# Kernel optimization log

Hardware: AMD Instinct MI355X
Metric: run time of the kernel (lower is better)

Reference implementation:

```python
import jax, jax.numpy as jnp
import numpy as np

N_NODES = 50000
N_EDGES = 1600000
F = 128
UNITS = 128


def leaky_relu2(x):
    # kgcnn>leaky_relu2: leaky relu with alpha=0.2
    return jnp.where(x > 0, x, 0.2 * x)


def glorot(key, shape):
    lim = np.sqrt(6.0 / (shape[0] + shape[1]))
    return jax.random.uniform(key, shape, jnp.float32, -lim, lim)


def setup_inputs() -> dict:
    key = jax.random.key(0)
    ks = jax.random.split(key, 8)
    node = jax.random.normal(ks[0], (N_NODES, F), jnp.float32)
    edge = jax.random.normal(ks[1], (N_EDGES, F), jnp.float32)
    edge_index = jax.random.randint(ks[2], (N_EDGES, 2), 0, N_NODES, jnp.int64)
    # lay_linear_trafo: Dense(units) on sender features
    W_lin = glorot(ks[3], (F, UNITS))
    b_lin = jnp.zeros((UNITS,), jnp.float32)
    # lay_alpha_activation: Dense(units, leaky_relu2) on concat [n_in || n_out]
    W_att = glorot(ks[4], (2 * F, UNITS))
    b_att = jnp.zeros((UNITS,), jnp.float32)
    # lay_alpha: Dense(1, linear, no bias)
    w_alpha = glorot(ks[5], (UNITS, 1))
    return {"node": node, "edge": edge, "edge_index": edge_index,
            "W_lin": W_lin, "b_lin": b_lin, "W_att": W_att, "b_att": b_att,
            "w_alpha": w_alpha}


def reference(node, edge, edge_index, W_lin, b_lin, W_att, b_att, w_alpha):
    recv = edge_index[:, 0]  # ingoing node i (receiver)
    send = edge_index[:, 1]  # outgoing node j (sender)
    n_in = node[recv]        # [M, F]
    n_out = node[send]       # [M, F]
    # linear trafo of sender features: W2 h_j
    wn_out = n_out @ W_lin + b_lin                       # [M, U]
    # attention logits a_ij = sigma1(W1 [h_i || h_j]) -> Dense(1)
    e_ij = leaky_relu2(jnp.concatenate([n_in, n_out], axis=-1) @ W_att + b_att)
    a_ij = (e_ij @ w_alpha)[:, 0]                        # [M]
    # segment softmax over edges incoming to each receiver node
    seg_max = jax.ops.segment_max(a_ij, recv, num_segments=N_NODES)
    seg_max = jnp.where(jnp.isfinite(seg_max), seg_max, 0.0)
    a_exp = jnp.exp(a_ij - seg_max[recv])
    denom = jax.ops.segment_sum(a_exp, recv, num_segments=N_NODES)
    alpha = a_exp / jnp.maximum(denom[recv], 1e-12)      # [M]
    # scatter weighted sum back to receiver nodes
    n_i = jax.ops.segment_sum(alpha[:, None] * wn_out, recv, num_segments=N_NODES)
    return jax.nn.elu(n_i)                               # [N, U]
```

## Files before the change

kernel.cpp:

```cpp
#include <hip/hip_runtime.h>
#include <hip/hip_bf16.h>
#include <math.h>

#define F 128
#define CAP 128

typedef __attribute__((ext_vector_type(8))) short bf16x8;
typedef __attribute__((ext_vector_type(4))) float f32x4;

static __device__ __forceinline__ unsigned short f2bf(float f) {
  unsigned u = __float_as_uint(f);
  unsigned r = (u + 0x7fffu + ((u >> 16) & 1u)) >> 16;
  return (unsigned short)r;
}
static __device__ __forceinline__ float bf2f(unsigned short h) {
  return __uint_as_float(((unsigned)h) << 16);
}

__global__ __launch_bounds__(256) void prep_kernel(
    const float* __restrict__ W_att, const float* __restrict__ W_lin,
    unsigned short* __restrict__ Bpack, int* __restrict__ deg, int nNodes) {
  const int i = blockIdx.x * 256 + threadIdx.x;
  if (i < nNodes) deg[i] = 0;
  if (i < 24 * 4 * 64 * 8) {
    const int j  = i & 7;
    const int l  = (i >> 3) & 63;
    const int kt = (i >> 9) & 3;
    const int ct = i >> 11;
    const int k = kt * 32 + ((l >> 4) << 3) + j;
    const int c = ct * 16 + (l & 15);
    float v;
    if (c < 128)      v = W_att[k * 128 + c];
    else if (c < 256) v = W_att[(k + 128) * 128 + (c - 128)];
    else              v = W_lin[k * 128 + (c - 256)];
    Bpack[i] = f2bf(v);
  }
}

static __device__ void gemm_body_mfma(
    int r0, const float* __restrict__ node,
    const unsigned short* __restrict__ Bpack,
    const float* __restrict__ b_att, const float* __restrict__ b_lin,
    float* __restrict__ A_in, unsigned short* __restrict__ P, int nNodes) {
  const int w   = threadIdx.x >> 6;
  const int l   = threadIdx.x & 63;
  const int l15 = l & 15;
  const int g   = l >> 4;

  const int rowA  = r0 + w * 16 + l15;
  const int rowAc = min(rowA, nNodes - 1);

  bf16x8 af[4];
  const float* arow = node + (size_t)rowAc * F + (g << 3);
#pragma unroll
  for (int kt = 0; kt < 4; ++kt) {
    const float4 x0 = *(const float4*)(arow + kt * 32);
    const float4 x1 = *(const float4*)(arow + kt * 32 + 4);
    bf16x8 a;
    a[0] = (short)f2bf(x0.x); a[1] = (short)f2bf(x0.y);
    a[2] = (short)f2bf(x0.z); a[3] = (short)f2bf(x0.w);
    a[4] = (short)f2bf(x1.x); a[5] = (short)f2bf(x1.y);
    a[6] = (short)f2bf(x1.z); a[7] = (short)f2bf(x1.w);
    af[kt] = a;
  }

  const int growBase = r0 + w * 16 + (g << 2);

  for (int ct = 0; ct < 24; ++ct) {
    f32x4 acc = {0.f, 0.f, 0.f, 0.f};
    const unsigned short* bp = Bpack + (((size_t)(ct * 4) * 64 + l) << 3);
#pragma unroll
    for (int kt = 0; kt < 4; ++kt) {
      const bf16x8 bfr = *(const bf16x8*)(bp + (kt << 9));
      acc = __builtin_amdgcn_mfma_f32_16x16x32_bf16(af[kt], bfr, acc, 0, 0, 0);
    }
    const int col = ct * 16 + l15;
#pragma unroll
    for (int r = 0; r < 4; ++r) {
      const int grow = growBase + r;
      if (grow < nNodes) {
        if (col < 128) {
          A_in[(size_t)grow * F + col] = acc[r] + b_att[col];
        } else if (col < 256) {
          P[(size_t)grow * 256 + (col - 128)] = f2bf(acc[r]);
        } else {
          P[(size_t)grow * 256 + 128 + (col - 256)] =
              f2bf(acc[r] + b_lin[col - 256]);
        }
      }
    }
  }
}

__global__ __launch_bounds__(256) void combo_kernel(
    const int2* __restrict__ ei2, int* __restrict__ deg,
    int* __restrict__ sorted_send, int nEdges, int SB,
    const float* __restrict__ node, const unsigned short* __restrict__ Bpack,
    const float* __restrict__ b_att, const float* __restrict__ b_lin,
    float* __restrict__ A_in, unsigned short* __restrict__ P, int nNodes) {
  if ((int)blockIdx.x < SB) {
    for (int e = (int)blockIdx.x * 256 + threadIdx.x; e < nEdges;
         e += SB * 256) {
      int2 p = ei2[e];
      int r = atomicAdd(&deg[p.x], 1);
      if (r < CAP) sorted_send[((size_t)p.x << 7) + r] = p.y;
    }
    return;
  }
  gemm_body_mfma((blockIdx.x - SB) * 64, node, Bpack, b_att, b_lin,
                 A_in, P, nNodes);
}

__global__ __launch_bounds__(256) void fused_node(
    const float* __restrict__ A_in, const unsigned short* __restrict__ P,
    const float* __restrict__ w_alpha, const int* __restrict__ deg,
    const int* __restrict__ sorted_send,
    float* __restrict__ out, int nNodes) {
  const int node = blockIdx.x * 4 + (threadIdx.x >> 6);
  const int lane = threadIdx.x & 63;
  if (node >= nNodes) return;

  const int e0 = node << 7;
  const int d  = min(deg[node], CAP);
  const int e1 = e0 + d;
  const int l31 = lane & 31;
  const int hi8 = (lane & 32) >> 2;
  const size_t no = (size_t)node * F;

  const float4 ai = *(const float4*)&A_in[no + (l31 << 2)];
  const float4 wa = *(const float4*)&w_alpha[l31 << 2];

  float4 acc = {0.f, 0.f, 0.f, 0.f};
  float pacc = 0.f;
  float tsave = 0.f;

  for (int base64 = e0; base64 < e1; base64 += 64) {
    const int myidx = (base64 + lane < e1) ? sorted_send[base64 + lane] : 0;
    const int rem = e1 - base64;
    const int nch = ((rem < 64 ? rem : 64) + 15) >> 4;
    for (int c = 0; c < nch; ++c) {
      const int base = base64 + c * 16;

      int srow[8];
      ushort4 qa[8], wb[8];
#pragma unroll
      for (int q = 0; q < 8; ++q) {
        srow[q] = __shfl(myidx, c * 16 + q + hi8);
        const unsigned short* rp = P + (size_t)srow[q] * 256 + (l31 << 2);
        qa[q] = *(const ushort4*)rp;
        wb[q] = *(const ushort4*)(rp + 128);
      }

#pragma unroll
      for (int q = 0; q < 8; ++q) {
        float x0 = bf2f(qa[q].x) + ai.x; x0 = fmaxf(x0, 0.2f * x0);
        float x1 = bf2f(qa[q].y) + ai.y; x1 = fmaxf(x1, 0.2f * x1);
        float x2 = bf2f(qa[q].z) + ai.z; x2 = fmaxf(x2, 0.2f * x2);
        float x3 = bf2f(qa[q].w) + ai.w; x3 = fmaxf(x3, 0.2f * x3);
        float s = fmaf(x0, wa.x, fmaf(x1, wa.y, fmaf(x2, wa.z, x3 * wa.w)));
        s += __shfl_xor(s, 1);
        s += __shfl_xor(s, 2);
        s += __shfl_xor(s, 4);
        s += __shfl_xor(s, 8);
        s += __shfl_xor(s, 16);
        tsave = (l31 == q) ? s : tsave;
      }

      const int edge = base + l31 + hi8;
      const float p = ((l31 < 8) && (edge < e1)) ? __expf(tsave) : 0.f;
      pacc += p;

#pragma unroll
      for (int q = 0; q < 8; ++q) {
        const float pq = __shfl(p, (lane & 32) + q);
        acc.x = fmaf(bf2f(wb[q].x), pq, acc.x);
        acc.y = fmaf(bf2f(wb[q].y), pq, acc.y);
        acc.z = fmaf(bf2f(wb[q].z), pq, acc.z);
        acc.w = fmaf(bf2f(wb[q].w), pq, acc.w);
      }
    }
  }

  acc.x += __shfl_xor(acc.x, 32);
  acc.y += __shfl_xor(acc.y, 32);
  acc.z += __shfl_xor(acc.z, 32);
  acc.w += __shfl_xor(acc.w, 32);
  for (int off = 1; off < 64; off <<= 1) pacc += __shfl_xor(pacc, off);

  const float inv = 1.f / fmaxf(pacc, 1e-12f);
  if (lane < 32) {
    float v0 = acc.x * inv, v1 = acc.y * inv, v2 = acc.z * inv, v3 = acc.w * inv;
    v0 = (v0 > 0.f) ? v0 : expm1f(v0);
    v1 = (v1 > 0.f) ? v1 : expm1f(v1);
    v2 = (v2 > 0.f) ? v2 : expm1f(v2);
    v3 = (v3 > 0.f) ? v3 : expm1f(v3);
    *(float4*)&out[no + (l31 << 2)] = float4{v0, v1, v2, v3};
  }
}

extern "C" void kernel_launch(void* const* d_in, const int* in_sizes, int n_in,
                              void* d_out, int out_size, void* d_ws, size_t ws_size,
                              hipStream_t stream) {
  const float* node    = (const float*)d_in[0];
  const int*   ei      = (const int*)d_in[2];
  const float* W_lin   = (const float*)d_in[3];
  const float* b_lin   = (const float*)d_in[4];
  const float* W_att   = (const float*)d_in[5];
  const float* b_att   = (const float*)d_in[6];
  const float* w_alpha = (const float*)d_in[7];

  const int nNodes = in_sizes[0] / F;
  const int nEdges = in_sizes[2] / 2;

  float* ws = (float*)d_ws;
  const size_t nf = (size_t)nNodes * F;
  float*          A_in = ws;
  unsigned short* P    = (unsigned short*)(ws + nf);
  int*            deg  = (int*)(ws + 2 * nf);
  int*  sorted_send    = deg + nNodes;
  unsigned short* Bpack =
      (unsigned short*)(sorted_send + (size_t)nNodes * CAP);

  const int PB = max((nNodes + 255) / 256, 192);
  const int SB = 768;
  const int GB = (nNodes + 63) / 64;
  const int NB = (nNodes + 3) / 4;

  prep_kernel<<<PB, 256, 0, stream>>>(W_att, W_lin, Bpack, deg, nNodes);
  combo_kernel<<<SB + GB, 256, 0, stream>>>(
      (const int2*)ei, deg, sorted_send, nEdges, SB,
      node, Bpack, b_att, b_lin, A_in, P, nNodes);
  fused_node<<<NB, 256, 0, stream>>>(
      A_in, P, w_alpha, deg, sorted_send, (float*)d_out, nNodes);
}
```

Baseline: 225.8 us.

## Double-buffer gathered edge rows in fused_node to overlap loads with compute

Restructures the per-node edge loop into a software pipeline with two register buffers. The next chunk's gathered P rows are issued before the current chunk's attention logits and weighted sum are computed. Both 64-index blocks of sorted_send are preloaded up front, replacing the nested 64/16 loop. This is meant to hide gather latency behind compute, at the cost of more registers and possibly lower occupancy.

Result: no change. 227.6 us (+0.8%).

```diff
diff --git a/kernel.cpp b/kernel.cpp
--- a/kernel.cpp
+++ b/kernel.cpp
@@ -122,7 +122,6 @@
 
   const int e0 = node << 7;
   const int d  = min(deg[node], CAP);
-  const int e1 = e0 + d;
   const int l31 = lane & 31;
   const int hi8 = (lane & 32) >> 2;
   const size_t no = (size_t)node * F;
@@ -133,53 +132,92 @@
   float4 acc = {0.f, 0.f, 0.f, 0.f};
   float pacc = 0.f;
   float tsave = 0.f;
-
-  for (int base64 = e0; base64 < e1; base64 += 64) {
-    const int myidx = (base64 + lane < e1) ? sorted_send[base64 + lane] : 0;
-    const int rem = e1 - base64;
-    const int nch = ((rem < 64 ? rem : 64) + 15) >> 4;
-    for (int c = 0; c < nch; ++c) {
-      const int base = base64 + c * 16;
-
-      int srow[8];
-      ushort4 qa[8], wb[8];
-#pragma unroll
-      for (int q = 0; q < 8; ++q) {
-        srow[q] = __shfl(myidx, c * 16 + q + hi8);
-        const unsigned short* rp = P + (size_t)srow[q] * 256 + (l31 << 2);
-        qa[q] = *(const ushort4*)rp;
-        wb[q] = *(const ushort4*)(rp + 128);
-      }
-
-#pragma unroll
-      for (int q = 0; q < 8; ++q) {
-        float x0 = bf2f(qa[q].x) + ai.x; x0 = fmaxf(x0, 0.2f * x0);
-        float x1 = bf2f(qa[q].y) + ai.y; x1 = fmaxf(x1, 0.2f * x1);
-        float x2 = bf2f(qa[q].z) + ai.z; x2 = fmaxf(x2, 0.2f * x2);
-        float x3 = bf2f(qa[q].w) + ai.w; x3 = fmaxf(x3, 0.2f * x3);
-        float s = fmaf(x0, wa.x, fmaf(x1, wa.y, fmaf(x2, wa.z, x3 * wa.w)));
-        s += __shfl_xor(s, 1);
-        s += __shfl_xor(s, 2);
-        s += __shfl_xor(s, 4);
-        s += __shfl_xor(s, 8);
-        s += __shfl_xor(s, 16);
-        tsave = (l31 == q) ? s : tsave;
-      }
-
-      const int edge = base + l31 + hi8;
-      const float p = ((l31 < 8) && (edge < e1)) ? __expf(tsave) : 0.f;
-      pacc += p;
-
-#pragma unroll
-      for (int q = 0; q < 8; ++q) {
-        const float pq = __shfl(p, (lane & 32) + q);
-        acc.x = fmaf(bf2f(wb[q].x), pq, acc.x);
-        acc.y = fmaf(bf2f(wb[q].y), pq, acc.y);
-        acc.z = fmaf(bf2f(wb[q].z), pq, acc.z);
-        acc.w = fmaf(bf2f(wb[q].w), pq, acc.w);
-      }
-    }
-  }
+  float p = 0.f;
+
+  const int myidx0 = (lane < d) ? sorted_send[e0 + lane] : 0;
+  const int myidx1 = (64 + lane < d) ? sorted_send[e0 + 64 + lane] : 0;
+
+  const int nch = (d + 15) >> 4;
+
+  ushort4 qaA[8], wbA[8], qaB[8], wbB[8];
+
+#define IDS(CH) (((CH) & 4) ? myidx1 : myidx0)
+
+#define ISSUE_QA(BUF, CH)                                              \
+  {                                                                    \
+    const int ids_ = IDS(CH);                                          \
+    _Pragma("unroll") for (int q = 0; q < 8; ++q) {                    \
+      const int srow = __shfl(ids_, ((CH) & 3) * 16 + q + hi8);        \
+      BUF[q] = *(const ushort4*)(P + (size_t)srow * 256 + (l31 << 2)); \
+    }                                                                  \
+  }
+
+#define ISSUE_WB(BUF, CH)                                              \
+  {                                                                    \
+    const int ids_ = IDS(CH);                                          \
+    _Pragma("unroll") for (int q = 0; q < 8; ++q) {                    \
+      const int srow = __shfl(ids_, ((CH) & 3) * 16 + q + hi8);        \
+      BUF[q] =                                                         \
+          *(const ushort4*)(P + (size_t)srow * 256 + 128 + (l31 << 2)); \
+    }                                                                  \
+  }
+
+#define PHASE_A(BUF, CH)                                               \
+  {                                                                    \
+    _Pragma("unroll") for (int q = 0; q < 8; ++q) {                    \
+      float x0 = bf2f(BUF[q].x) + ai.x; x0 = fmaxf(x0, 0.2f * x0);     \
+      float x1 = bf2f(BUF[q].y) + ai.y; x1 = fmaxf(x1, 0.2f * x1);     \
+      float x2 = bf2f(BUF[q].z) + ai.z; x2 = fmaxf(x2, 0.2f * x2);     \
+      float x3 = bf2f(BUF[q].w) + ai.w; x3 = fmaxf(x3, 0.2f * x3);     \
+      float s = fmaf(x0, wa.x, fmaf(x1, wa.y, fmaf(x2, wa.z, x3 * wa.w))); \
+      s += __shfl_xor(s, 1);                                           \
+      s += __shfl_xor(s, 2);                                           \
+      s += __shfl_xor(s, 4);                                           \
+      s += __shfl_xor(s, 8);                                           \
+      s += __shfl_xor(s, 16);                                          \
+      tsave = (l31 == q) ? s : tsave;                                  \
+    }                                                                  \
+    const int edge = (CH) * 16 + l31 + hi8;                            \
+    p = ((l31 < 8) && (edge < d)) ? __expf(tsave) : 0.f;               \
+    pacc += p;                                                         \
+  }
+
+#define PHASE_B(BUF)                                                   \
+  {                                                                    \
+    _Pragma("unroll") for (int q = 0; q < 8; ++q) {                    \
+      const float pq = __shfl(p, (lane & 32) + q);                     \
+      acc.x = fmaf(bf2f(BUF[q].x), pq, acc.x);                         \
+      acc.y = fmaf(bf2f(BUF[q].y), pq, acc.y);                         \
+      acc.z = fmaf(bf2f(BUF[q].z), pq, acc.z);                         \
+      acc.w = fmaf(bf2f(BUF[q].w), pq, acc.w);                         \
+    }                                                                  \
+  }
+
+  if (nch > 0) {
+    ISSUE_QA(qaA, 0);
+    ISSUE_WB(wbA, 0);
+    int ch = 0;
+    for (; ch + 2 <= nch; ch += 2) {
+      ISSUE_QA(qaB, ch + 1);
+      PHASE_A(qaA, ch);
+      ISSUE_WB(wbB, ch + 1);
+      PHASE_B(wbA);
+      if (ch + 2 < nch) ISSUE_QA(qaA, ch + 2);
+      PHASE_A(qaB, ch + 1);
+      if (ch + 2 < nch) ISSUE_WB(wbA, ch + 2);
+      PHASE_B(wbB);
+    }
+    if (ch < nch) {
+      PHASE_A(qaA, ch);
+      PHASE_B(wbA);
+    }
+  }
+
+#undef IDS
+#undef ISSUE_QA
+#undef ISSUE_WB
+#undef PHASE_A
+#undef PHASE_B
 
   acc.x += __shfl_xor(acc.x, 32);
   acc.y += __shfl_xor(acc.y, 32);
```
